# Kernel optimization log

Hardware: AMD Instinct MI355X
Metric: run time of the kernel (lower is better)

The kernel has to match this reference:

```python
import jax, jax.numpy as jnp
import numpy as np

NB_HEAD = 4
SIZE_PER_HEAD = 50
D_MODEL = 200
B, S = 4, 4096


def setup_inputs() -> dict:
    key = jax.random.key(0)
    ks = jax.random.split(key, 7)
    q = jax.random.normal(ks[0], (B, S, D_MODEL), dtype=jnp.float32)
    k = jax.random.normal(ks[1], (B, S, D_MODEL), dtype=jnp.float32)
    v = jax.random.normal(ks[2], (B, S, D_MODEL), dtype=jnp.float32)
    # glorot-uniform-like init for weights
    def glorot(key, shape):
        lim = jnp.sqrt(6.0 / (shape[0] + shape[1])).astype(jnp.float32)
        return jax.random.uniform(key, shape, jnp.float32, -lim, lim)
    WQ = glorot(ks[3], (D_MODEL, SIZE_PER_HEAD))
    WK = glorot(ks[4], (D_MODEL, SIZE_PER_HEAD))
    WV = glorot(ks[5], (D_MODEL, SIZE_PER_HEAD))
    WO = glorot(ks[6], (NB_HEAD * SIZE_PER_HEAD, D_MODEL))
    return {"q": q, "k": k, "v": v, "WQ": WQ, "WK": WK, "WV": WV, "WO": WO}


def reference(q, k, v, WQ, WK, WV, WO):
    # The original per-head loop reuses the SAME WQ/WK/WV each iteration,
    # so every head output is identical. Compute attention once and tile.
    Qp = jnp.einsum('bsd,de->bse', q, WQ)  # [B,S,h]
    Kp = jnp.einsum('bsd,de->bse', k, WK)
    Vp = jnp.einsum('bsd,de->bse', v, WV)
    scale = 1.0 / jnp.sqrt(jnp.asarray(SIZE_PER_HEAD, dtype=Qp.dtype))
    A = jax.nn.softmax(jnp.einsum('bqe,bke->bqk', Qp, Kp) * scale, axis=-1)  # [B,S,S]
    O = jnp.einsum('bqk,bke->bqe', A, Vp)  # [B,S,h]
    O_concat = jnp.tile(O, (1, 1, NB_HEAD))  # [B,S,NB_HEAD*h]
    return jnp.einsum('bsf,fd->bsd', O_concat, WO)
```

## Files before the change

### kernel.cpp

```cpp
#include <hip/hip_runtime.h>
#include <hip/hip_bf16.h>


typedef short s4 __attribute__((ext_vector_type(4)));
typedef short s8 __attribute__((ext_vector_type(8)));
typedef float f4 __attribute__((ext_vector_type(4)));
typedef unsigned u2 __attribute__((ext_vector_type(2)));

#define SLEN 4096
#define NB 4
#define DMODEL 200
#define HREAL 50
#define HP 64
#define DMP 208
#define XPAD 212
#define KVB 64
#define QSCALE 0.20402789f

__device__ __forceinline__ short f2bf(float f) {
  unsigned u = __builtin_bit_cast(unsigned, f);
  u += 0x7FFFu + ((u >> 16) & 1u);
  return (short)(u >> 16);
}

__device__ __forceinline__ float bf2f(short s) {
  unsigned u = ((unsigned)(unsigned short)s) << 16;
  return __builtin_bit_cast(float, u);
}

__device__ __forceinline__ float fexp2(float x) { return __builtin_amdgcn_exp2f(x); }

__global__ void prep_weights(const float* __restrict__ WQ, const float* __restrict__ WK,
                             const float* __restrict__ WV, const float* __restrict__ WO,
                             short* __restrict__ wqt, short* __restrict__ wkt,
                             short* __restrict__ wvt, short* __restrict__ wot) {
  int id = blockIdx.x * 256 + threadIdx.x;
  const int NW = HP * DMP;
  if (id < 3 * NW) {
    int which = id / NW, rem = id % NW;
    int e = rem / DMP, d = rem % DMP;
    float v = 0.f;
    if (e < HREAL && d < DMODEL) {
      const float* W = (which == 0) ? WQ : (which == 1 ? WK : WV);
      v = W[d * HREAL + e];
      if (which == 0) v *= QSCALE;
    }
    short* T = (which == 0) ? wqt : (which == 1 ? wkt : wvt);
    T[e * DMP + d] = f2bf(v);
  } else if (id < 4 * NW) {
    int rem = id - 3 * NW;
    int dm = rem / HP, e = rem % HP;
    float v = 0.f;
    if (dm < DMODEL && e < HREAL) {
      v = WO[(e)*DMODEL + dm] + WO[(HREAL + e) * DMODEL + dm] +
          WO[(2 * HREAL + e) * DMODEL + dm] + WO[(3 * HREAL + e) * DMODEL + dm];
    }
    wot[dm * HP + e] = f2bf(v);
  }
}

__global__ __launch_bounds__(256) void proj_kernel(
    const float* __restrict__ q, const float* __restrict__ k, const float* __restrict__ v,
    const short* __restrict__ wqt, const short* __restrict__ wkt, const short* __restrict__ wvt,
    short* __restrict__ Qp, short* __restrict__ Kp, short* __restrict__ VpT) {
  __shared__ __align__(16) short Xl[64 * XPAD];
  __shared__ __align__(16) short Wl[64 * XPAD];
  const int mode = blockIdx.z;
  const float* X = (mode == 0) ? q : (mode == 1 ? k : v);
  const short* WT = (mode == 0) ? wqt : (mode == 1 ? wkt : wvt);
  const int tid = threadIdx.x;
  const int sb64 = blockIdx.x * 64;

  {
    const f4* src = (const f4*)(X + (size_t)sb64 * DMODEL);
#pragma unroll
    for (int i = 0; i < 13; ++i) {
      int idx = tid + i * 256;
      if (idx < 3200) {
        f4 a = src[idx];
        int row = idx / 50, c = idx - row * 50;
        s4 bv;
#pragma unroll
        for (int j = 0; j < 4; ++j) bv[j] = f2bf(a[j]);
        *(s4*)(Xl + row * XPAD + c * 4) = bv;
      }
    }
    if (tid < 192) {
      int row = tid / 3, c = 200 + (tid - (tid / 3) * 3) * 4;
      s4 z = {0, 0, 0, 0};
      *(s4*)(Xl + row * XPAD + c) = z;
    }
    const s8* wsrc = (const s8*)WT;
#pragma unroll
    for (int i = 0; i < 7; ++i) {
      int idx = tid + i * 256;
      if (idx < 1664) {
        s8 wc = wsrc[idx];
        int row = idx / 26, c8 = idx - row * 26;
        s4 lo = {wc[0], wc[1], wc[2], wc[3]};
        s4 hi = {wc[4], wc[5], wc[6], wc[7]};
        *(s4*)(Wl + row * XPAD + c8 * 8) = lo;
        *(s4*)(Wl + row * XPAD + c8 * 8 + 4) = hi;
      }
    }
  }
  __syncthreads();

  const int lane = tid & 63, wid = tid >> 6;
  const int l15 = lane & 15, g = lane >> 4;
  const int row16 = wid * 16 + l15;
  const int sbase = sb64 + wid * 16;
  f4 acc[4] = {};
#pragma unroll
  for (int c = 0; c < 13; ++c) {
    int d0 = 16 * c + 4 * g;
    s4 af = *(const s4*)(Xl + row16 * XPAD + d0);
#pragma unroll
    for (int n = 0; n < 4; ++n) {
      s4 bf = *(const s4*)(Wl + (16 * n + l15) * XPAD + d0);
      acc[n] = __builtin_amdgcn_mfma_f32_16x16x16bf16_1k(af, bf, acc[n], 0, 0, 0);
    }
  }
  if (mode < 2) {
    short* OUT = (mode == 0) ? Qp : Kp;
#pragma unroll
    for (int n = 0; n < 4; ++n)
#pragma unroll
      for (int r = 0; r < 4; ++r) {
        int rr = sbase + 4 * g + r;
        OUT[rr * HP + 16 * n + l15] = f2bf(acc[n][r]);
      }
  } else {
#pragma unroll
    for (int n = 0; n < 4; ++n)
#pragma unroll
      for (int r = 0; r < 4; ++r) {
        int rr = sbase + 4 * g + r;
        int bb = rr >> 12, s = rr & 4095;
        VpT[((bb * HP) + 16 * n + l15) * SLEN + s] = f2bf(acc[n][r]);
      }
  }
}

__global__ __launch_bounds__(256, 4) void attn_kernel(
    const short* __restrict__ Qp, const short* __restrict__ Kp,
    const short* __restrict__ VpT, float* __restrict__ Mp,
    float* __restrict__ Lp, short* __restrict__ Opb) {
  __shared__ __align__(16) char Klds[2][KVB * 128];
  __shared__ __align__(16) char Vlds[2][HP * 128];
  const int tid = threadIdx.x;
  const int lane = tid & 63, wid = tid >> 6;
  const int l15 = lane & 15, g = lane >> 4;
  const int b = blockIdx.y, z = blockIdx.z;
  const int nsplit = gridDim.z;
  const int qrowA = blockIdx.x * 128 + wid * 32 + l15;
  const int qrowB = qrowA + 16;
  const int ksw = (l15 & 7) << 4;

  s8 qfA[2], qfB[2];
  {
    const short* qpa = Qp + (size_t)(b * SLEN + qrowA) * HP + 8 * g;
    const short* qpb = Qp + (size_t)(b * SLEN + qrowB) * HP + 8 * g;
    qfA[0] = *(const s8*)(qpa);
    qfA[1] = *(const s8*)(qpa + 32);
    qfB[0] = *(const s8*)(qpb);
    qfB[1] = *(const s8*)(qpb + 32);
  }

  const int kr0 = l15 * 128 + ((16 * g) ^ ksw);
  const int kr1 = l15 * 128 + ((64 + 16 * g) ^ ksw);
  const int vb = l15 * 128 + ((8 * g) ^ ksw);

  const int cj0 = tid, cj1 = tid + 256;
  const int ci0 = (cj0 ^ ((cj0 >> 3) & 7)) * 16;
  const int ci1 = (cj1 ^ ((cj1 >> 3) & 7)) * 16;
  const int d0 = cj0 >> 3, d1 = cj1 >> 3;
  const int ch0 = ((cj0 & 7) ^ (d0 & 7)) * 16;
  const int ch1 = ((cj1 & 7) ^ (d1 & 7)) * 16;

  const int kv0 = z * (SLEN / nsplit);
  const char* kp0 = (const char*)Kp + (size_t)(b * SLEN + kv0) * 128 + ci0;
  const char* kp1 = (const char*)Kp + (size_t)(b * SLEN + kv0) * 128 + ci1;
  const char* vp0 =
      (const char*)VpT + ((size_t)(b * HP + d0) * SLEN + kv0) * 2 + ch0;
  const char* vp1 =
      (const char*)VpT + ((size_t)(b * HP + d1) * SLEN + kv0) * 2 + ch1;

  {
    f4 k0 = *(const f4*)kp0;
    f4 k1 = *(const f4*)kp1;
    f4 v0 = *(const f4*)vp0;
    f4 v1 = *(const f4*)vp1;
    *(f4*)(Klds[0] + tid * 16) = k0;
    *(f4*)(Klds[0] + tid * 16 + 4096) = k1;
    *(f4*)(Vlds[0] + tid * 16) = v0;
    *(f4*)(Vlds[0] + tid * 16 + 4096) = v1;
    kp0 += KVB * 128;
    kp1 += KVB * 128;
    vp0 += KVB * 2;
    vp1 += KVB * 2;
  }

  f4 oA[4] = {}, oB[4] = {};
  float mA = -1e30f, lsumA = 0.f;
  float mB = -1e30f, lsumB = 0.f;
  const int nsteps = SLEN / nsplit / KVB;
  for (int step = 0; step < nsteps; ++step) {
    const int p = step & 1;
    f4 rk0, rk1, rv0, rv1;
    const bool more = (step + 1 < nsteps);
    if (more) {
      rk0 = *(const f4*)kp0;
      rk1 = *(const f4*)kp1;
      rv0 = *(const f4*)vp0;
      rv1 = *(const f4*)vp1;
      kp0 += KVB * 128;
      kp1 += KVB * 128;
      vp0 += KVB * 2;
      vp1 += KVB * 2;
    }
    __syncthreads();
    const char* Kbuf = Klds[p];
    const char* Vbuf = Vlds[p];
#pragma unroll
    for (int tt = 0; tt < 4; ++tt) {
      f4 stA = {}, stB = {};
      {
        s8 kf0 = *(const s8*)(Kbuf + kr0 + tt * 2048);
        s8 kf1 = *(const s8*)(Kbuf + kr1 + tt * 2048);
        __builtin_amdgcn_s_setprio(1);
        stA = __builtin_amdgcn_mfma_f32_16x16x32_bf16(kf0, qfA[0], stA, 0, 0, 0);
        stB = __builtin_amdgcn_mfma_f32_16x16x32_bf16(kf0, qfB[0], stB, 0, 0, 0);
        stA = __builtin_amdgcn_mfma_f32_16x16x32_bf16(kf1, qfA[1], stA, 0, 0, 0);
        stB = __builtin_amdgcn_mfma_f32_16x16x32_bf16(kf1, qfB[1], stB, 0, 0, 0);
        __builtin_amdgcn_s_setprio(0);
      }
      float tmaxA = fmaxf(fmaxf(stA[0], stA[1]), fmaxf(stA[2], stA[3]));
      if (__builtin_expect(__any(tmaxA > mA + 8.0f), 0)) {
        float t = fmaxf(tmaxA, __shfl_xor(tmaxA, 16));
        t = fmaxf(t, __shfl_xor(t, 32));
        t = fmaxf(t, mA);
        float corr = fexp2(mA - t);
        lsumA *= corr;
#pragma unroll
        for (int n = 0; n < 4; ++n) {
          oA[n][0] *= corr; oA[n][1] *= corr; oA[n][2] *= corr; oA[n][3] *= corr;
        }
        mA = t;
      }
      float pa0 = fexp2(stA[0] - mA), pa1 = fexp2(stA[1] - mA);
      float pa2 = fexp2(stA[2] - mA), pa3 = fexp2(stA[3] - mA);
      lsumA += (pa0 + pa1) + (pa2 + pa3);
      union { unsigned u[2]; s4 s; } puA;
      asm("v_cvt_pk_bf16_f32 %0, %1, %2" : "=v"(puA.u[0]) : "v"(pa0), "v"(pa1));
      asm("v_cvt_pk_bf16_f32 %0, %1, %2" : "=v"(puA.u[1]) : "v"(pa2), "v"(pa3));
      s4 pfA = puA.s;
      float tmaxB = fmaxf(fmaxf(stB[0], stB[1]), fmaxf(stB[2], stB[3]));
      if (__builtin_expect(__any(tmaxB > mB + 8.0f), 0)) {
        float t = fmaxf(tmaxB, __shfl_xor(tmaxB, 16));
        t = fmaxf(t, __shfl_xor(t, 32));
        t = fmaxf(t, mB);
        float corr = fexp2(mB - t);
        lsumB *= corr;
#pragma unroll
        for (int n = 0; n < 4; ++n) {
          oB[n][0] *= corr; oB[n][1] *= corr; oB[n][2] *= corr; oB[n][3] *= corr;
        }
        mB = t;
      }
      float pb0 = fexp2(stB[0] - mB), pb1 = fexp2(stB[1] - mB);
      float pb2 = fexp2(stB[2] - mB), pb3 = fexp2(stB[3] - mB);
      lsumB += (pb0 + pb1) + (pb2 + pb3);
      union { unsigned u[2]; s4 s; } puB;
      asm("v_cvt_pk_bf16_f32 %0, %1, %2" : "=v"(puB.u[0]) : "v"(pb0), "v"(pb1));
      asm("v_cvt_pk_bf16_f32 %0, %1, %2" : "=v"(puB.u[1]) : "v"(pb2), "v"(pb3));
      s4 pfB = puB.s;
      const char* vrow = Vbuf + (vb ^ (tt << 5));
      __builtin_amdgcn_s_setprio(1);
#pragma unroll
      for (int n = 0; n < 4; ++n) {
        s4 vf = *(const s4*)(vrow + n * 2048);
        oA[n] = __builtin_amdgcn_mfma_f32_16x16x16bf16_1k(vf, pfA, oA[n], 0, 0, 0);
        oB[n] = __builtin_amdgcn_mfma_f32_16x16x16bf16_1k(vf, pfB, oB[n], 0, 0, 0);
      }
      __builtin_amdgcn_s_setprio(0);
    }
    if (more) {
      *(f4*)(Klds[p ^ 1] + tid * 16) = rk0;
      *(f4*)(Klds[p ^ 1] + tid * 16 + 4096) = rk1;
      *(f4*)(Vlds[p ^ 1] + tid * 16) = rv0;
      *(f4*)(Vlds[p ^ 1] + tid * 16 + 4096) = rv1;
    }
  }
  lsumA += __shfl_xor(lsumA, 16);
  lsumA += __shfl_xor(lsumA, 32);
  lsumB += __shfl_xor(lsumB, 16);
  lsumB += __shfl_xor(lsumB, 32);
  const int rowgA = b * SLEN + qrowA;
  const int rowgB = b * SLEN + qrowB;
  const int NR = NB * SLEN;
  if (lane < 16) {
    Mp[z * NR + rowgA] = mA;
    Lp[z * NR + rowgA] = lsumA;
    Mp[z * NR + rowgB] = mB;
    Lp[z * NR + rowgB] = lsumB;
  }
  short* opA = Opb + ((size_t)z * NR + rowgA) * HP;
  short* opB = Opb + ((size_t)z * NR + rowgB) * HP;
#pragma unroll
  for (int n = 0; n < 4; ++n) {
    u2 ua, ub;
    asm("v_cvt_pk_bf16_f32 %0, %1, %2" : "=v"(ua[0]) : "v"(oA[n][0]), "v"(oA[n][1]));
    asm("v_cvt_pk_bf16_f32 %0, %1, %2" : "=v"(ua[1]) : "v"(oA[n][2]), "v"(oA[n][3]));
    asm("v_cvt_pk_bf16_f32 %0, %1, %2" : "=v"(ub[0]) : "v"(oB[n][0]), "v"(oB[n][1]));
    asm("v_cvt_pk_bf16_f32 %0, %1, %2" : "=v"(ub[1]) : "v"(oB[n][2]), "v"(oB[n][3]));
    *(u2*)(opA + 16 * n + 4 * g) = ua;
    *(u2*)(opB + 16 * n + 4 * g) = ub;
  }
}

template <int NSPLIT>
__global__ __launch_bounds__(256) void combineproj_kernel(
    const float* __restrict__ Mp, const float* __restrict__ Lp,
    const short* __restrict__ Opb, const short* __restrict__ wot,
    float* __restrict__ out) {
  const int lane = threadIdx.x & 63, wid = threadIdx.x >> 6;
  const int l15 = lane & 15, g = lane >> 4;
  const int sbase = blockIdx.x * 64 + wid * 16;
  const int row = sbase + l15;
  const int NR = NB * SLEN;
  float mm = -1e30f;
#pragma unroll
  for (int s = 0; s < NSPLIT; ++s) mm = fmaxf(mm, Mp[s * NR + row]);
  float w[NSPLIT];
  float L = 0.f;
#pragma unroll
  for (int s = 0; s < NSPLIT; ++s) {
    w[s] = fexp2(Mp[s * NR + row] - mm);
    L += w[s] * Lp[s * NR + row];
  }
  float inv = 1.0f / L;
  s4 af[4];
#pragma unroll
  for (int c = 0; c < 4; ++c) {
    f4 acc = {};
#pragma unroll
    for (int s = 0; s < NSPLIT; ++s) {
      s4 sv = *(const s4*)(Opb + ((size_t)s * NR + row) * HP + 16 * c + 4 * g);
      acc[0] += w[s] * bf2f(sv[0]);
      acc[1] += w[s] * bf2f(sv[1]);
      acc[2] += w[s] * bf2f(sv[2]);
      acc[3] += w[s] * bf2f(sv[3]);
    }
#pragma unroll
    for (int r = 0; r < 4; ++r) af[c][r] = f2bf(acc[r] * inv);
  }
  for (int n = 0; n < 13; ++n) {
    f4 acc = {};
    const short* brow = wot + (16 * n + l15) * HP + 4 * g;
#pragma unroll
    for (int c = 0; c < 4; ++c) {
      s4 bf = *(const s4*)(brow + 16 * c);
      acc = __builtin_amdgcn_mfma_f32_16x16x16bf16_1k(af[c], bf, acc, 0, 0, 0);
    }
    int dm = 16 * n + l15;
    if (dm < DMODEL) {
#pragma unroll
      for (int r = 0; r < 4; ++r) {
        int rr = sbase + 4 * g + r;
        out[(size_t)rr * DMODEL + dm] = acc[r];
      }
    }
  }
}

extern "C" void kernel_launch(void* const* d_in, const int* in_sizes, int n_in,
                              void* d_out, int out_size, void* d_ws, size_t ws_size,
                              hipStream_t stream) {
  const float* q = (const float*)d_in[0];
  const float* k = (const float*)d_in[1];
  const float* v = (const float*)d_in[2];
  const float* WQ = (const float*)d_in[3];
  const float* WK = (const float*)d_in[4];
  const float* WV = (const float*)d_in[5];
  const float* WO = (const float*)d_in[6];
  float* out = (float*)d_out;
  char* ws = (char*)d_ws;

  const size_t MB2 = 2097152;
  const size_t NR = (size_t)NB * SLEN;
  auto need = [&](int n) {
    return (size_t)131072 + 3 * MB2 + (size_t)n * NR * 4 * 2 + (size_t)n * NR * HP * 2;
  };
  int nsplit = (ws_size >= need(8)) ? 8 : 4;

  short* wqt = (short*)(ws + 0);
  short* wkt = (short*)(ws + 32768);
  short* wvt = (short*)(ws + 65536);
  short* wot = (short*)(ws + 98304);
  short* Qp = (short*)(ws + 131072);
  short* Kp = (short*)(ws + 131072 + MB2);
  short* VpT = (short*)(ws + 131072 + 2 * MB2);
  float* Mp = (float*)(ws + 131072 + 3 * MB2);
  float* Lp = Mp + nsplit * NR;
  short* Opb = (short*)(Lp + nsplit * NR);

  prep_weights<<<dim3(208), dim3(256), 0, stream>>>(WQ, WK, WV, WO, wqt, wkt, wvt, wot);
  proj_kernel<<<dim3(256, 1, 3), dim3(256), 0, stream>>>(q, k, v, wqt, wkt, wvt, Qp, Kp, VpT);
  attn_kernel<<<dim3(32, NB, nsplit), dim3(256), 0, stream>>>(Qp, Kp, VpT, Mp, Lp, Opb);
  if (nsplit == 8)
    combineproj_kernel<8><<<dim3(256), dim3(256), 0, stream>>>(Mp, Lp, Opb, wot, out);
  else
    combineproj_kernel<4><<<dim3(256), dim3(256), 0, stream>>>(Mp, Lp, Opb, wot, out);
}
```

Measured before the change: 66.17 us.

## Fold weight prep into projection kernel and software-pipeline QK MFMAs

Removes the separate prep_weights launch. Each projection block now reads and transposes the fp32 Q/K/V weights straight into LDS, and a fourth grid slice builds the head-summed WO. In the attention inner loop, the QK score MFMAs for the next 16-key sub-tile are issued before the softmax and PV work of the current one, so MFMA latency can overlap with the exp math. The cost is that every projection block redoes the weight transpose with strided LDS stores, and the pipelined loop needs more registers.

```diff
diff --git a/kernel.cpp b/kernel.cpp
--- a/kernel.cpp
+++ b/kernel.cpp
@@ -30,45 +30,30 @@
 
 __device__ __forceinline__ float fexp2(float x) { return __builtin_amdgcn_exp2f(x); }
 
-__global__ void prep_weights(const float* __restrict__ WQ, const float* __restrict__ WK,
-                             const float* __restrict__ WV, const float* __restrict__ WO,
-                             short* __restrict__ wqt, short* __restrict__ wkt,
-                             short* __restrict__ wvt, short* __restrict__ wot) {
-  int id = blockIdx.x * 256 + threadIdx.x;
-  const int NW = HP * DMP;
-  if (id < 3 * NW) {
-    int which = id / NW, rem = id % NW;
-    int e = rem / DMP, d = rem % DMP;
-    float v = 0.f;
-    if (e < HREAL && d < DMODEL) {
-      const float* W = (which == 0) ? WQ : (which == 1 ? WK : WV);
-      v = W[d * HREAL + e];
-      if (which == 0) v *= QSCALE;
-    }
-    short* T = (which == 0) ? wqt : (which == 1 ? wkt : wvt);
-    T[e * DMP + d] = f2bf(v);
-  } else if (id < 4 * NW) {
-    int rem = id - 3 * NW;
-    int dm = rem / HP, e = rem % HP;
-    float v = 0.f;
-    if (dm < DMODEL && e < HREAL) {
-      v = WO[(e)*DMODEL + dm] + WO[(HREAL + e) * DMODEL + dm] +
-          WO[(2 * HREAL + e) * DMODEL + dm] + WO[(3 * HREAL + e) * DMODEL + dm];
-    }
-    wot[dm * HP + e] = f2bf(v);
-  }
-}
-
 __global__ __launch_bounds__(256) void proj_kernel(
     const float* __restrict__ q, const float* __restrict__ k, const float* __restrict__ v,
-    const short* __restrict__ wqt, const short* __restrict__ wkt, const short* __restrict__ wvt,
-    short* __restrict__ Qp, short* __restrict__ Kp, short* __restrict__ VpT) {
+    const float* __restrict__ WQ, const float* __restrict__ WK, const float* __restrict__ WV,
+    const float* __restrict__ WO, short* __restrict__ Qp, short* __restrict__ Kp,
+    short* __restrict__ VpT, short* __restrict__ wot) {
+  const int mode = blockIdx.z;
+  const int tid = threadIdx.x;
+  if (mode == 3) {
+    int id = blockIdx.x * 256 + tid;
+    if (blockIdx.x < 52 && id < DMP * HP) {
+      int dm = id / HP, e = id % HP;
+      float vv = 0.f;
+      if (dm < DMODEL && e < HREAL) {
+        vv = WO[(e)*DMODEL + dm] + WO[(HREAL + e) * DMODEL + dm] +
+             WO[(2 * HREAL + e) * DMODEL + dm] + WO[(3 * HREAL + e) * DMODEL + dm];
+      }
+      wot[dm * HP + e] = f2bf(vv);
+    }
+    return;
+  }
   __shared__ __align__(16) short Xl[64 * XPAD];
   __shared__ __align__(16) short Wl[64 * XPAD];
-  const int mode = blockIdx.z;
   const float* X = (mode == 0) ? q : (mode == 1 ? k : v);
-  const short* WT = (mode == 0) ? wqt : (mode == 1 ? wkt : wvt);
-  const int tid = threadIdx.x;
+  const float* Wsrc = (mode == 0) ? WQ : (mode == 1 ? WK : WV);
   const int sb64 = blockIdx.x * 64;
 
   {
@@ -90,17 +75,23 @@
       s4 z = {0, 0, 0, 0};
       *(s4*)(Xl + row * XPAD + c) = z;
     }
-    const s8* wsrc = (const s8*)WT;
-#pragma unroll
-    for (int i = 0; i < 7; ++i) {
+    s4 z = {0, 0, 0, 0};
+#pragma unroll
+    for (int i = 0; i < 14; ++i) {
       int idx = tid + i * 256;
-      if (idx < 1664) {
-        s8 wc = wsrc[idx];
-        int row = idx / 26, c8 = idx - row * 26;
-        s4 lo = {wc[0], wc[1], wc[2], wc[3]};
-        s4 hi = {wc[4], wc[5], wc[6], wc[7]};
-        *(s4*)(Wl + row * XPAD + c8 * 8) = lo;
-        *(s4*)(Wl + row * XPAD + c8 * 8 + 4) = hi;
+      if (idx < (64 * XPAD) / 4) *(s4*)(Wl + idx * 4) = z;
+    }
+  }
+  __syncthreads();
+  {
+#pragma unroll
+    for (int i = 0; i < 40; ++i) {
+      int flat = tid + i * 256;
+      if (flat < DMODEL * HREAL) {
+        float vv = Wsrc[flat];
+        int d = flat / HREAL, e = flat - HREAL * d;
+        if (mode == 0) vv *= QSCALE;
+        Wl[e * XPAD + d] = f2bf(vv);
       }
     }
   }
@@ -222,17 +213,28 @@
     __syncthreads();
     const char* Kbuf = Klds[p];
     const char* Vbuf = Vlds[p];
+    f4 stA, stB;
+    {
+      s8 kf0 = *(const s8*)(Kbuf + kr0);
+      s8 kf1 = *(const s8*)(Kbuf + kr1);
+      __builtin_amdgcn_s_setprio(1);
+      stA = __builtin_amdgcn_mfma_f32_16x16x32_bf16(kf0, qfA[0], (f4){}, 0, 0, 0);
+      stB = __builtin_amdgcn_mfma_f32_16x16x32_bf16(kf0, qfB[0], (f4){}, 0, 0, 0);
+      stA = __builtin_amdgcn_mfma_f32_16x16x32_bf16(kf1, qfA[1], stA, 0, 0, 0);
+      stB = __builtin_amdgcn_mfma_f32_16x16x32_bf16(kf1, qfB[1], stB, 0, 0, 0);
+      __builtin_amdgcn_s_setprio(0);
+    }
 #pragma unroll
     for (int tt = 0; tt < 4; ++tt) {
-      f4 stA = {}, stB = {};
-      {
-        s8 kf0 = *(const s8*)(Kbuf + kr0 + tt * 2048);
-        s8 kf1 = *(const s8*)(Kbuf + kr1 + tt * 2048);
+      f4 stA2, stB2;
+      if (tt < 3) {
+        s8 kf0 = *(const s8*)(Kbuf + kr0 + (tt + 1) * 2048);
+        s8 kf1 = *(const s8*)(Kbuf + kr1 + (tt + 1) * 2048);
         __builtin_amdgcn_s_setprio(1);
-        stA = __builtin_amdgcn_mfma_f32_16x16x32_bf16(kf0, qfA[0], stA, 0, 0, 0);
-        stB = __builtin_amdgcn_mfma_f32_16x16x32_bf16(kf0, qfB[0], stB, 0, 0, 0);
-        stA = __builtin_amdgcn_mfma_f32_16x16x32_bf16(kf1, qfA[1], stA, 0, 0, 0);
-        stB = __builtin_amdgcn_mfma_f32_16x16x32_bf16(kf1, qfB[1], stB, 0, 0, 0);
+        stA2 = __builtin_amdgcn_mfma_f32_16x16x32_bf16(kf0, qfA[0], (f4){}, 0, 0, 0);
+        stB2 = __builtin_amdgcn_mfma_f32_16x16x32_bf16(kf0, qfB[0], (f4){}, 0, 0, 0);
+        stA2 = __builtin_amdgcn_mfma_f32_16x16x32_bf16(kf1, qfA[1], stA2, 0, 0, 0);
+        stB2 = __builtin_amdgcn_mfma_f32_16x16x32_bf16(kf1, qfB[1], stB2, 0, 0, 0);
         __builtin_amdgcn_s_setprio(0);
       }
       float tmaxA = fmaxf(fmaxf(stA[0], stA[1]), fmaxf(stA[2], stA[3]));
@@ -284,6 +286,10 @@
         oB[n] = __builtin_amdgcn_mfma_f32_16x16x16bf16_1k(vf, pfB, oB[n], 0, 0, 0);
       }
       __builtin_amdgcn_s_setprio(0);
+      if (tt < 3) {
+        stA = stA2;
+        stB = stB2;
+      }
     }
     if (more) {
       *(f4*)(Klds[p ^ 1] + tid * 16) = rk0;
@@ -394,9 +400,6 @@
   };
   int nsplit = (ws_size >= need(8)) ? 8 : 4;
 
-  short* wqt = (short*)(ws + 0);
-  short* wkt = (short*)(ws + 32768);
-  short* wvt = (short*)(ws + 65536);
   short* wot = (short*)(ws + 98304);
   short* Qp = (short*)(ws + 131072);
   short* Kp = (short*)(ws + 131072 + MB2);
@@ -405,8 +408,8 @@
   float* Lp = Mp + nsplit * NR;
   short* Opb = (short*)(Lp + nsplit * NR);
 
-  prep_weights<<<dim3(208), dim3(256), 0, stream>>>(WQ, WK, WV, WO, wqt, wkt, wvt, wot);
-  proj_kernel<<<dim3(256, 1, 3), dim3(256), 0, stream>>>(q, k, v, wqt, wkt, wvt, Qp, Kp, VpT);
+  proj_kernel<<<dim3(256, 1, 4), dim3(256), 0, stream>>>(q, k, v, WQ, WK, WV, WO,
+                                                          Qp, Kp, VpT, wot);
   attn_kernel<<<dim3(32, NB, nsplit), dim3(256), 0, stream>>>(Qp, Kp, VpT, Mp, Lp, Opb);
   if (nsplit == 8)
     combineproj_kernel<8><<<dim3(256), dim3(256), 0, stream>>>(Mp, Lp, Opb, wot, out);
```

Measured after the change: 64.81 us. 2.1% less time.
